# Performance work log

Measured on AMD Instinct MI355X. Metric: run time of the kernel, lower is better.

The kernel has to match this reference:

```python
import jax, jax.numpy as jnp
import numpy as np

B, D, FV, EMB, HID, E = 256, 1000, 300, 128, 128, 32000
NUM_LAYERS = 3


def _gcn_layer(h, src, tgt, W, b):
    # PyG GCNConv (add_self_loops=True, normalize=True) over N = h.shape[0] nodes.
    # NOTE: edges only reference nodes [0, D) (faithful to original forward),
    # but self-loops exist for all N nodes.
    N = h.shape[0]
    h = h @ W.T  # [N, out]
    deg = jnp.ones((N,), h.dtype).at[tgt].add(1.0)  # self-loop + in-degree
    dinv = deg ** -0.5
    coef = dinv[src] * dinv[tgt]  # [E]
    agg = jnp.zeros_like(h).at[tgt].add(h[src] * coef[:, None])
    agg = agg + h * (dinv * dinv)[:, None]  # self-loop messages
    return agg + b


def setup_inputs() -> dict:
    key = jax.random.key(0)
    ks = jax.random.split(key, 10)
    inp = {
        "X_num": jax.random.normal(ks[0], (B, 800), jnp.float32),
        "X_cat": jax.random.normal(ks[1], (B, 200), jnp.float32),
        "V": jax.random.normal(ks[2], (D, FV), jnp.float32),
        "edge_index": jax.random.randint(ks[3], (2, E), 0, D, jnp.int32),
        "W_embed": jax.random.normal(ks[4], (EMB, FV), jnp.float32) / np.sqrt(FV),
        "b_embed": jnp.zeros((EMB,), jnp.float32),
        "W0": jax.random.normal(ks[5], (HID, EMB), jnp.float32) / np.sqrt(EMB),
        "b0": jnp.zeros((HID,), jnp.float32),
        "W1": jax.random.normal(ks[6], (HID, HID), jnp.float32) / np.sqrt(HID),
        "b1": jnp.zeros((HID,), jnp.float32),
        "W2": jax.random.normal(ks[7], (HID, HID), jnp.float32) / np.sqrt(HID),
        "b2": jnp.zeros((HID,), jnp.float32),
    }
    return inp


def reference(X_num, X_cat, V, edge_index, W_embed, b_embed, W0, b0, W1, b1, W2, b2):
    x = jnp.concatenate([X_num, X_cat], axis=1)  # [B, D]
    emb = V @ W_embed.T + b_embed  # [D, EMB]
    h = x[:, :, None] * emb[None, :, :]  # [B, D, EMB]
    h = h.reshape(B * D, EMB)
    src, tgt = edge_index[0], edge_index[1]
    for W, b in ((W0, b0), (W1, b1), (W2, b2)):
        h = jax.nn.relu(_gcn_layer(h, src, tgt, W, b))
    h = h.reshape(B, D, HID)
    return h.mean(axis=1)  # conv_pool_method == 'mean'
```

## Files before the change

### kernel.cpp

```cpp
#include <hip/hip_runtime.h>

#define B_N 256
#define D_N 1000
#define H_N 128
#define E_N 32000
#define CAP 128

typedef unsigned int uint32;
typedef unsigned short u16;
typedef __attribute__((ext_vector_type(8))) short bf16x8;
typedef __attribute__((ext_vector_type(4))) float f32x4;

__device__ __forceinline__ u16 f2bf(float f) {
    union { float f; uint32 u; } v; v.f = f;
    return (u16)((v.u + 0x7fffu + ((v.u >> 16) & 1u)) >> 16);
}
__device__ __forceinline__ float bf2f(u16 h) {
    union { uint32 u; float f; } v; v.u = ((uint32)h) << 16;
    return v.f;
}

__global__ void k_setup(const float* __restrict__ V, const float* __restrict__ W_embed,
                        const float* __restrict__ b_embed, const int* __restrict__ eidx,
                        const float* __restrict__ W1, const float* __restrict__ W2,
                        int* deg, int* __restrict__ es,
                        u16* __restrict__ w1h, u16* __restrict__ w2h,
                        float* __restrict__ emb) {
    int bid = blockIdx.x, tid = threadIdx.x;
    if (bid < 500) {
        __shared__ float sV[600];
        for (int i = tid; i < 600; i += 256) sV[i] = V[bid * 600 + i];
        __syncthreads();
        int half = tid >> 7, e = tid & 127;
        int d = bid * 2 + half;
        const float4* wr = (const float4*)(W_embed + e * 300);
        const float4* vv = (const float4*)(sV + half * 300);
        float s = b_embed[e];
#pragma unroll 5
        for (int f = 0; f < 75; ++f) {
            float4 w = wr[f], x = vv[f];
            s += w.x * x.x + w.y * x.y + w.z * x.z + w.w * x.w;
        }
        emb[d * H_N + e] = s;
    } else if (bid < 625) {
        int e = (bid - 500) * 256 + tid;
        if (e < E_N) {
            int s = eidx[e], t = eidx[E_N + e];
            int pos = atomicAdd(&deg[t], 1);
            if (pos < CAP) es[t * CAP + pos] = s;
        }
    } else {
        int i = (bid - 625) * 256 + tid;
        if (i < H_N * H_N) { w1h[i] = f2bf(W1[i]); w2h[i] = f2bf(W2[i]); }
    }
}

__global__ void k_e1(const float* __restrict__ emb, const float* __restrict__ W0,
                     const float* __restrict__ Xn, const float* __restrict__ Xc,
                     const int* __restrict__ deg, u16* __restrict__ E1h,
                     float* __restrict__ t0, float* __restrict__ dinv) {
    __shared__ float se[256];
    int tid = threadIdx.x, bid = blockIdx.x;
    se[tid] = emb[bid * 256 + tid];
    if (tid < 2) {
        int dd = bid * 2 + tid;
        dinv[dd] = rsqrtf(1.0f + (float)deg[dd]);
    }
    __syncthreads();
    int half = tid >> 7, e = tid & 127;
    int d = bid * 2 + half;
    const float4* er = (const float4*)(se + half * 128);
    const float4* wr = (const float4*)(W0 + e * 128);
    float s = 0.f;
#pragma unroll 8
    for (int k = 0; k < 32; ++k) {
        float4 a = er[k], w = wr[k];
        s += a.x * w.x + a.y * w.y + a.z * w.z + a.w * w.w;
    }
    E1h[d * H_N + e] = f2bf(s);
    float x0 = (d < 800) ? Xn[d] : Xc[d - 800];
    t0[d * H_N + e] = x0 * s;
}

__global__ void k_layer(const float* __restrict__ t_in, const float* __restrict__ bias,
                        const float* __restrict__ Wn, const int* __restrict__ deg,
                        const int* __restrict__ es, const float* __restrict__ dinv,
                        float* __restrict__ t_out, float* out, int pool) {
    __shared__ float sh[128];
    int d = blockIdx.x, e = threadIdx.x;
    float di = dinv[d];
    float acc = t_in[d * H_N + e] * di * di;
    int n = deg[d]; if (n > CAP) n = CAP;
    const int* row = es + d * CAP;
    for (int i = 0; i < n; ++i) {
        int s = row[i];
        acc += di * dinv[s] * t_in[s * H_N + e];
    }
    float h = acc + bias[e];
    h = h > 0.f ? h : 0.f;
    if (pool) { atomicAdd(&out[e], h * (1.0f / 1000.0f)); return; }
    sh[e] = h;
    __syncthreads();
    const float4* hr = (const float4*)sh;
    const float4* wr = (const float4*)(Wn + e * 128);
    float s = 0.f;
#pragma unroll 8
    for (int k = 0; k < 32; ++k) {
        float4 a = hr[k], w = wr[k];
        s += a.x * w.x + a.y * w.y + a.z * w.z + a.w * w.w;
    }
    t_out[d * H_N + e] = s;
}

__device__ __forceinline__ int swzo(int row, int col) {
    return row * 128 + ((((col >> 3) ^ (row & 7))) << 3) + (col & 7);
}

__global__ __launch_bounds__(256, 1)
void k_big(const float* __restrict__ Xn, const float* __restrict__ Xc,
           const u16* __restrict__ E1h, const u16* __restrict__ w1h,
           const u16* __restrict__ w2h, const float* __restrict__ b0,
           const float* __restrict__ b1, const float* __restrict__ b2,
           float* __restrict__ out) {
    __shared__ __align__(16) u16 sH[4 * 32 * 128];
    const int tid = threadIdx.x;
    const int wave = tid >> 6, lane = tid & 63;
    const int quad = lane >> 4, l15 = lane & 15;
    const int bi = 1 + blockIdx.x;
    u16* wbase = sH + wave * (32 * 128);

    bf16x8 w1f[8][4], w2f[8][4];
#pragma unroll
    for (int n = 0; n < 8; ++n)
#pragma unroll
        for (int ks = 0; ks < 4; ++ks) {
            int off = (n * 16 + l15) * 128 + (ks * 4 + quad) * 8;
            w1f[n][ks] = *(const bf16x8*)(w1h + off);
            w2f[n][ks] = *(const bf16x8*)(w2h + off);
        }

    uint32 b0p[4][4];
#pragma unroll
    for (int ks = 0; ks < 4; ++ks) {
        const float* bp = b0 + (ks * 4 + quad) * 8;
#pragma unroll
        for (int q = 0; q < 4; ++q)
            b0p[ks][q] = (uint32)f2bf(bp[2 * q]) | ((uint32)f2bf(bp[2 * q + 1]) << 16);
    }
    float b1g[8], b2g[8];
#pragma unroll
    for (int n = 0; n < 8; ++n) { b1g[n] = b1[n * 16 + l15]; b2g[n] = b2[n * 16 + l15]; }

    float accO[8];
#pragma unroll
    for (int n = 0; n < 8; ++n) accO[n] = 0.f;

    const int odd = l15 & 1;

    for (int c = 0; c < 8; ++c) {
        int tile = wave * 8 + c;
        int mbase = tile * 32;

        float xv[2];
#pragma unroll
        for (int rt = 0; rt < 2; ++rt) {
            int m = mbase + rt * 16 + l15;
            int mc = m < D_N ? m : D_N - 1;
            xv[rt] = (mc < 800) ? Xn[bi * 800 + mc] : Xc[bi * 200 + (mc - 800)];
        }

        uint4 e1r[4][2];
#pragma unroll
        for (int ks = 0; ks < 4; ++ks)
#pragma unroll
            for (int rt = 0; rt < 2; ++rt) {
                int m = mbase + rt * 16 + l15;
                int mc = m < D_N ? m : D_N - 1;
                e1r[ks][rt] = *(const uint4*)(E1h + mc * H_N + (ks * 4 + quad) * 8);
            }

        f32x4 acc[2][8];
#pragma unroll
        for (int rt = 0; rt < 2; ++rt)
#pragma unroll
            for (int n = 0; n < 8; ++n) { acc[rt][n][0] = 0.f; acc[rt][n][1] = 0.f; acc[rt][n][2] = 0.f; acc[rt][n][3] = 0.f; }

#pragma unroll
        for (int ks = 0; ks < 4; ++ks) {
            bf16x8 a[2];
#pragma unroll
            for (int rt = 0; rt < 2; ++rt) {
                const u16* ep = (const u16*)&e1r[ks][rt];
                bf16x8 av;
#pragma unroll
                for (int j = 0; j < 8; ++j) {
                    float bb = bf2f((u16)((b0p[ks][j >> 1] >> ((j & 1) * 16)) & 0xffffu));
                    float h = xv[rt] * bf2f(ep[j]) + bb;
                    h = h > 0.f ? h : 0.f;
                    av[j] = (short)f2bf(h);
                }
                a[rt] = av;
            }
#pragma unroll
            for (int n = 0; n < 8; ++n) {
                acc[0][n] = __builtin_amdgcn_mfma_f32_16x16x32_bf16(a[0], w1f[n][ks], acc[0][n], 0, 0, 0);
                acc[1][n] = __builtin_amdgcn_mfma_f32_16x16x32_bf16(a[1], w1f[n][ks], acc[1][n], 0, 0, 0);
            }
        }

#pragma unroll
        for (int rt = 0; rt < 2; ++rt)
#pragma unroll
            for (int n = 0; n < 8; ++n) {
                float v0 = acc[rt][n][0] + b1g[n]; v0 = v0 > 0.f ? v0 : 0.f;
                float v1 = acc[rt][n][1] + b1g[n]; v1 = v1 > 0.f ? v1 : 0.f;
                float v2 = acc[rt][n][2] + b1g[n]; v2 = v2 > 0.f ? v2 : 0.f;
                float v3 = acc[rt][n][3] + b1g[n]; v3 = v3 > 0.f ? v3 : 0.f;
                float t0 = __shfl_xor(v0, 1), t1 = __shfl_xor(v1, 1);
                float t2 = __shfl_xor(v2, 1), t3 = __shfl_xor(v3, 1);
                float lo0 = odd ? t2 : v0, hi0 = odd ? v2 : t0;
                float lo1 = odd ? t3 : v1, hi1 = odd ? v3 : t1;
                int rA = rt * 16 + quad * 4 + (odd ? 2 : 0);
                int ce = n * 16 + (l15 & ~1);
                uint32 p0 = (uint32)f2bf(lo0) | ((uint32)f2bf(hi0) << 16);
                uint32 p1 = (uint32)f2bf(lo1) | ((uint32)f2bf(hi1) << 16);
                *(uint32*)&wbase[swzo(rA, ce)] = p0;
                *(uint32*)&wbase[swzo(rA + 1, ce)] = p1;
            }
        __syncthreads();

#pragma unroll
        for (int rt = 0; rt < 2; ++rt)
#pragma unroll
            for (int n = 0; n < 8; ++n) { acc[rt][n][0] = 0.f; acc[rt][n][1] = 0.f; acc[rt][n][2] = 0.f; acc[rt][n][3] = 0.f; }
#pragma unroll
        for (int ks = 0; ks < 4; ++ks) {
            bf16x8 a2[2];
#pragma unroll
            for (int rt = 0; rt < 2; ++rt) {
                int r = rt * 16 + l15;
                a2[rt] = *(const bf16x8*)&wbase[r * 128 + (((ks * 4 + quad) ^ (r & 7)) << 3)];
            }
#pragma unroll
            for (int n = 0; n < 8; ++n) {
                acc[0][n] = __builtin_amdgcn_mfma_f32_16x16x32_bf16(a2[0], w2f[n][ks], acc[0][n], 0, 0, 0);
                acc[1][n] = __builtin_amdgcn_mfma_f32_16x16x32_bf16(a2[1], w2f[n][ks], acc[1][n], 0, 0, 0);
            }
        }

        int rem = D_N - mbase;
#pragma unroll
        for (int rt = 0; rt < 2; ++rt)
#pragma unroll
            for (int n = 0; n < 8; ++n)
#pragma unroll
                for (int i = 0; i < 4; ++i) {
                    int row32 = rt * 16 + quad * 4 + i;
                    float v = acc[rt][n][i] + b2g[n];
                    v = v > 0.f ? v : 0.f;
                    if (row32 < rem) accO[n] += v;
                }
        __syncthreads();
    }

#pragma unroll
    for (int n = 0; n < 8; ++n) {
        float cs = accO[n];
        cs += __shfl_xor(cs, 16);
        cs += __shfl_xor(cs, 32);
        if (lane < 16) atomicAdd(&out[bi * H_N + n * 16 + l15], cs * (1.0f / 1000.0f));
    }
}

extern "C" void kernel_launch(void* const* d_in, const int* in_sizes, int n_in,
                              void* d_out, int out_size, void* d_ws, size_t ws_size,
                              hipStream_t stream) {
    const float* Xn = (const float*)d_in[0];
    const float* Xc = (const float*)d_in[1];
    const float* V = (const float*)d_in[2];
    const int* eidx = (const int*)d_in[3];
    const float* W_embed = (const float*)d_in[4];
    const float* b_embed = (const float*)d_in[5];
    const float* W0 = (const float*)d_in[6];
    const float* b0 = (const float*)d_in[7];
    const float* W1 = (const float*)d_in[8];
    const float* b1 = (const float*)d_in[9];
    const float* W2 = (const float*)d_in[10];
    const float* b2 = (const float*)d_in[11];
    float* out = (float*)d_out;

    char* p = (char*)d_ws;
    auto alloc = [&](size_t bytes) -> char* {
        char* r = p;
        p += (bytes + 255) & ~(size_t)255;
        return r;
    };
    float* emb  = (float*)alloc(D_N * H_N * 4);
    u16*   E1h  = (u16*)  alloc(D_N * H_N * 2);
    float* t0   = (float*)alloc(D_N * H_N * 4);
    float* t1   = (float*)alloc(D_N * H_N * 4);
    float* t2   = (float*)alloc(D_N * H_N * 4);
    u16*   w1h  = (u16*)  alloc(H_N * H_N * 2);
    u16*   w2h  = (u16*)  alloc(H_N * H_N * 2);
    float* dinv = (float*)alloc(D_N * 4);
    int*   deg  = (int*)  alloc(D_N * 4);
    int*   es   = (int*)  alloc(D_N * CAP * 4);

    hipMemsetAsync(deg, 0, D_N * 4, stream);
    hipMemsetAsync(out, 0, B_N * H_N * 4, stream);

    k_setup<<<dim3(689), dim3(256), 0, stream>>>(V, W_embed, b_embed, eidx, W1, W2,
                                                 deg, es, w1h, w2h, emb);
    k_e1<<<dim3(500), dim3(256), 0, stream>>>(emb, W0, Xn, Xc, deg, E1h, t0, dinv);
    k_big<<<dim3(255), dim3(256), 0, stream>>>(Xn, Xc, E1h, w1h, w2h, b0, b1, b2, out);
    k_layer<<<dim3(1000), dim3(128), 0, stream>>>(t0, b0, W1, deg, es, dinv, t1, out, 0);
    k_layer<<<dim3(1000), dim3(128), 0, stream>>>(t1, b1, W2, deg, es, dinv, t2, out, 0);
    k_layer<<<dim3(1000), dim3(128), 0, stream>>>(t2, b2, (const float*)nullptr, deg, es, dinv,
                                                  (float*)nullptr, out, 1);
}
```

Measured before the change: 222.2 us.

## Fuse setup and E1 kernels, split big kernel across two blocks per batch

Merges the embedding, W0 projection, edge bucketing, weight conversion and output zeroing into one prep kernel, which removes a launch and the memset of out. The layer kernel computes the inverse-sqrt degree inline and unrolls the neighbor gather by four. k_big now runs two blocks per batch row with a 2-blocks-per-CU launch bound. It keeps W1 in swizzled LDS and reads W2 fragments from global memory instead of holding both weight matrices in registers, and it drops the per-chunk barrier. This trades register pressure for more occupancy and parallelism, at the cost of repeated global or LDS reads of the weights.

```diff
diff --git a/kernel.cpp b/kernel.cpp
--- a/kernel.cpp
+++ b/kernel.cpp
@@ -1,4 +1,5 @@
 #include <hip/hip_runtime.h>
+#include <hip/hip_bf16.h>
 
 #define B_N 256
 #define D_N 1000
@@ -15,86 +16,98 @@
     union { float f; uint32 u; } v; v.f = f;
     return (u16)((v.u + 0x7fffu + ((v.u >> 16) & 1u)) >> 16);
 }
-__device__ __forceinline__ float bf2f(u16 h) {
-    union { uint32 u; float f; } v; v.u = ((uint32)h) << 16;
-    return v.f;
-}
-
-__global__ void k_setup(const float* __restrict__ V, const float* __restrict__ W_embed,
-                        const float* __restrict__ b_embed, const int* __restrict__ eidx,
-                        const float* __restrict__ W1, const float* __restrict__ W2,
-                        int* deg, int* __restrict__ es,
-                        u16* __restrict__ w1h, u16* __restrict__ w2h,
-                        float* __restrict__ emb) {
+__device__ __forceinline__ float asf(uint32 u) {
+    union { uint32 u; float f; } v; v.u = u; return v.f;
+}
+
+__global__ void k_prep(const float* __restrict__ V, const float* __restrict__ W_embed,
+                       const float* __restrict__ b_embed, const int* __restrict__ eidx,
+                       const float* __restrict__ W0,
+                       const float* __restrict__ Xn, const float* __restrict__ Xc,
+                       const float* __restrict__ W1, const float* __restrict__ W2,
+                       int* deg, int* __restrict__ es,
+                       u16* __restrict__ w1h, u16* __restrict__ w2h,
+                       u16* __restrict__ E1h, float* __restrict__ t0,
+                       float* __restrict__ out) {
     int bid = blockIdx.x, tid = threadIdx.x;
-    if (bid < 500) {
-        __shared__ float sV[600];
-        for (int i = tid; i < 600; i += 256) sV[i] = V[bid * 600 + i];
-        __syncthreads();
-        int half = tid >> 7, e = tid & 127;
-        int d = bid * 2 + half;
+    if (bid < 125) {
+        __shared__ float sEmb[8 * 128];
+        int e = tid & 127, h = tid >> 7;
+        int d0 = bid * 8 + h * 4;
         const float4* wr = (const float4*)(W_embed + e * 300);
-        const float4* vv = (const float4*)(sV + half * 300);
-        float s = b_embed[e];
+        float s0 = b_embed[e], s1 = s0, s2 = s0, s3 = s0;
 #pragma unroll 5
         for (int f = 0; f < 75; ++f) {
-            float4 w = wr[f], x = vv[f];
-            s += w.x * x.x + w.y * x.y + w.z * x.z + w.w * x.w;
-        }
-        emb[d * H_N + e] = s;
-    } else if (bid < 625) {
-        int e = (bid - 500) * 256 + tid;
-        if (e < E_N) {
-            int s = eidx[e], t = eidx[E_N + e];
-            int pos = atomicAdd(&deg[t], 1);
-            if (pos < CAP) es[t * CAP + pos] = s;
-        }
+            float4 w = wr[f];
+            float4 v0 = *(const float4*)(V + (d0 + 0) * 300 + f * 4);
+            float4 v1 = *(const float4*)(V + (d0 + 1) * 300 + f * 4);
+            float4 v2 = *(const float4*)(V + (d0 + 2) * 300 + f * 4);
+            float4 v3 = *(const float4*)(V + (d0 + 3) * 300 + f * 4);
+            s0 += w.x * v0.x + w.y * v0.y + w.z * v0.z + w.w * v0.w;
+            s1 += w.x * v1.x + w.y * v1.y + w.z * v1.z + w.w * v1.w;
+            s2 += w.x * v2.x + w.y * v2.y + w.z * v2.z + w.w * v2.w;
+            s3 += w.x * v3.x + w.y * v3.y + w.z * v3.z + w.w * v3.w;
+        }
+        sEmb[(h * 4 + 0) * 128 + e] = s0;
+        sEmb[(h * 4 + 1) * 128 + e] = s1;
+        sEmb[(h * 4 + 2) * 128 + e] = s2;
+        sEmb[(h * 4 + 3) * 128 + e] = s3;
+        __syncthreads();
+        const float4* w0r = (const float4*)(W0 + e * 128);
+        float t[4] = {0.f, 0.f, 0.f, 0.f};
+#pragma unroll 8
+        for (int k = 0; k < 32; ++k) {
+            float4 w = w0r[k];
+#pragma unroll
+            for (int p = 0; p < 4; ++p) {
+                float4 em = *(const float4*)&sEmb[(h * 4 + p) * 128 + k * 4];
+                t[p] += w.x * em.x + w.y * em.y + w.z * em.z + w.w * em.w;
+            }
+        }
+#pragma unroll
+        for (int p = 0; p < 4; ++p) {
+            int d = d0 + p;
+            float x0 = (d < 800) ? Xn[d] : Xc[d - 800];
+            E1h[d * H_N + e] = f2bf(t[p]);
+            t0[d * H_N + e] = x0 * t[p];
+        }
+    } else if (bid < 250) {
+        int i = (bid - 125) * 256 + tid;
+        int s = eidx[i], t = eidx[E_N + i];
+        int pos = atomicAdd(&deg[t], 1);
+        if (pos < CAP) es[t * CAP + pos] = s;
+    } else if (bid < 314) {
+        int i = (bid - 250) * 256 + tid;
+        w1h[i] = f2bf(W1[i]); w2h[i] = f2bf(W2[i]);
     } else {
-        int i = (bid - 625) * 256 + tid;
-        if (i < H_N * H_N) { w1h[i] = f2bf(W1[i]); w2h[i] = f2bf(W2[i]); }
-    }
-}
-
-__global__ void k_e1(const float* __restrict__ emb, const float* __restrict__ W0,
-                     const float* __restrict__ Xn, const float* __restrict__ Xc,
-                     const int* __restrict__ deg, u16* __restrict__ E1h,
-                     float* __restrict__ t0, float* __restrict__ dinv) {
-    __shared__ float se[256];
-    int tid = threadIdx.x, bid = blockIdx.x;
-    se[tid] = emb[bid * 256 + tid];
-    if (tid < 2) {
-        int dd = bid * 2 + tid;
-        dinv[dd] = rsqrtf(1.0f + (float)deg[dd]);
-    }
-    __syncthreads();
-    int half = tid >> 7, e = tid & 127;
-    int d = bid * 2 + half;
-    const float4* er = (const float4*)(se + half * 128);
-    const float4* wr = (const float4*)(W0 + e * 128);
-    float s = 0.f;
-#pragma unroll 8
-    for (int k = 0; k < 32; ++k) {
-        float4 a = er[k], w = wr[k];
-        s += a.x * w.x + a.y * w.y + a.z * w.z + a.w * w.w;
-    }
-    E1h[d * H_N + e] = f2bf(s);
-    float x0 = (d < 800) ? Xn[d] : Xc[d - 800];
-    t0[d * H_N + e] = x0 * s;
+        int i = (bid - 314) * 256 + tid;
+        out[i] = 0.f;
+    }
 }
 
 __global__ void k_layer(const float* __restrict__ t_in, const float* __restrict__ bias,
                         const float* __restrict__ Wn, const int* __restrict__ deg,
-                        const int* __restrict__ es, const float* __restrict__ dinv,
+                        const int* __restrict__ es,
                         float* __restrict__ t_out, float* out, int pool) {
     __shared__ float sh[128];
     int d = blockIdx.x, e = threadIdx.x;
-    float di = dinv[d];
+    float di = rsqrtf(1.f + (float)deg[d]);
     float acc = t_in[d * H_N + e] * di * di;
     int n = deg[d]; if (n > CAP) n = CAP;
     const int* row = es + d * CAP;
-    for (int i = 0; i < n; ++i) {
+    int i = 0;
+    for (; i + 4 <= n; i += 4) {
+        int a0 = row[i], a1 = row[i + 1], a2 = row[i + 2], a3 = row[i + 3];
+        float c0 = rsqrtf(1.f + (float)deg[a0]);
+        float c1 = rsqrtf(1.f + (float)deg[a1]);
+        float c2 = rsqrtf(1.f + (float)deg[a2]);
+        float c3 = rsqrtf(1.f + (float)deg[a3]);
+        acc += di * (c0 * t_in[a0 * H_N + e] + c1 * t_in[a1 * H_N + e] +
+                     c2 * t_in[a2 * H_N + e] + c3 * t_in[a3 * H_N + e]);
+    }
+    for (; i < n; ++i) {
         int s = row[i];
-        acc += di * dinv[s] * t_in[s * H_N + e];
+        acc += di * rsqrtf(1.f + (float)deg[s]) * t_in[s * H_N + e];
     }
     float h = acc + bias[e];
     h = h > 0.f ? h : 0.f;
@@ -112,155 +125,158 @@
     t_out[d * H_N + e] = s;
 }
 
-__device__ __forceinline__ int swzo(int row, int col) {
-    return row * 128 + ((((col >> 3) ^ (row & 7))) << 3) + (col & 7);
-}
-
-__global__ __launch_bounds__(256, 1)
+__device__ __forceinline__ int swz(int row, int col8) {
+    return row * 128 + ((col8 ^ (row & 7)) << 3);
+}
+
+__global__ __launch_bounds__(256, 2)
 void k_big(const float* __restrict__ Xn, const float* __restrict__ Xc,
            const u16* __restrict__ E1h, const u16* __restrict__ w1h,
            const u16* __restrict__ w2h, const float* __restrict__ b0,
            const float* __restrict__ b1, const float* __restrict__ b2,
            float* __restrict__ out) {
-    __shared__ __align__(16) u16 sH[4 * 32 * 128];
+    __shared__ __align__(16) u16 sW1[128 * 128];
+    __shared__ __align__(16) u16 sT[4 * 32 * 128];
+
     const int tid = threadIdx.x;
     const int wave = tid >> 6, lane = tid & 63;
     const int quad = lane >> 4, l15 = lane & 15;
-    const int bi = 1 + blockIdx.x;
-    u16* wbase = sH + wave * (32 * 128);
-
-    bf16x8 w1f[8][4], w2f[8][4];
-#pragma unroll
-    for (int n = 0; n < 8; ++n)
+    const int bi = 1 + (blockIdx.x >> 1);
+    const int half = blockIdx.x & 1;
+    u16* tw = sT + wave * (32 * 128);
+    const int odd = l15 & 1;
+
+    {
+        const uint4* src = (const uint4*)w1h;
+        for (int i = tid; i < 2048; i += 256) {
+            int row = i >> 4, g = i & 15;
+            *(uint4*)&sW1[swz(row, g)] = src[i];
+        }
+    }
+
+    float b0v[4][8];
+#pragma unroll
+    for (int ks = 0; ks < 4; ++ks) {
+        float4 lo = *(const float4*)(b0 + (ks * 4 + quad) * 8);
+        float4 hi = *(const float4*)(b0 + (ks * 4 + quad) * 8 + 4);
+        b0v[ks][0] = lo.x; b0v[ks][1] = lo.y; b0v[ks][2] = lo.z; b0v[ks][3] = lo.w;
+        b0v[ks][4] = hi.x; b0v[ks][5] = hi.y; b0v[ks][6] = hi.z; b0v[ks][7] = hi.w;
+    }
+    float b1g[8], b2g[8];
+#pragma unroll
+    for (int n = 0; n < 8; ++n) { b1g[n] = b1[n * 16 + l15]; b2g[n] = b2[n * 16 + l15]; }
+
+    __syncthreads();
+
+    float accO[8];
+#pragma unroll
+    for (int n = 0; n < 8; ++n) accO[n] = 0.f;
+
+    for (int c = 0; c < 4; ++c) {
+        int mbase = half * 512 + wave * 128 + c * 32;
+        int rA = mbase + l15;      int rAc = rA < D_N ? rA : D_N - 1;
+        int rB = rA + 16;          int rBc = rB < D_N ? rB : D_N - 1;
+        float xvA = (rAc < 800) ? Xn[bi * 800 + rAc] : Xc[bi * 200 + rAc - 800];
+        float xvB = (rBc < 800) ? Xn[bi * 800 + rBc] : Xc[bi * 200 + rBc - 800];
+
+        uint4 eA[4], eB[4];
 #pragma unroll
         for (int ks = 0; ks < 4; ++ks) {
-            int off = (n * 16 + l15) * 128 + (ks * 4 + quad) * 8;
-            w1f[n][ks] = *(const bf16x8*)(w1h + off);
-            w2f[n][ks] = *(const bf16x8*)(w2h + off);
-        }
-
-    uint32 b0p[4][4];
-#pragma unroll
-    for (int ks = 0; ks < 4; ++ks) {
-        const float* bp = b0 + (ks * 4 + quad) * 8;
-#pragma unroll
-        for (int q = 0; q < 4; ++q)
-            b0p[ks][q] = (uint32)f2bf(bp[2 * q]) | ((uint32)f2bf(bp[2 * q + 1]) << 16);
-    }
-    float b1g[8], b2g[8];
-#pragma unroll
-    for (int n = 0; n < 8; ++n) { b1g[n] = b1[n * 16 + l15]; b2g[n] = b2[n * 16 + l15]; }
-
-    float accO[8];
-#pragma unroll
-    for (int n = 0; n < 8; ++n) accO[n] = 0.f;
-
-    const int odd = l15 & 1;
-
-    for (int c = 0; c < 8; ++c) {
-        int tile = wave * 8 + c;
-        int mbase = tile * 32;
-
-        float xv[2];
+            eA[ks] = *(const uint4*)(E1h + rAc * H_N + (ks * 4 + quad) * 8);
+            eB[ks] = *(const uint4*)(E1h + rBc * H_N + (ks * 4 + quad) * 8);
+        }
+
+        f32x4 acc0[8], acc1[8];
+#pragma unroll
+        for (int n = 0; n < 8; ++n) {
+            acc0[n][0] = 0.f; acc0[n][1] = 0.f; acc0[n][2] = 0.f; acc0[n][3] = 0.f;
+            acc1[n][0] = 0.f; acc1[n][1] = 0.f; acc1[n][2] = 0.f; acc1[n][3] = 0.f;
+        }
+
+#pragma unroll
+        for (int ks = 0; ks < 4; ++ks) {
+            const uint32* pA = (const uint32*)&eA[ks];
+            const uint32* pB = (const uint32*)&eB[ks];
+            bf16x8 aA, aB;
+#pragma unroll
+            for (int p = 0; p < 4; ++p) {
+                uint32 uA = pA[p], uB = pB[p];
+                float hA0 = fmaf(xvA, asf(uA << 16), b0v[ks][2 * p]);
+                float hA1 = fmaf(xvA, asf(uA & 0xffff0000u), b0v[ks][2 * p + 1]);
+                float hB0 = fmaf(xvB, asf(uB << 16), b0v[ks][2 * p]);
+                float hB1 = fmaf(xvB, asf(uB & 0xffff0000u), b0v[ks][2 * p + 1]);
+                hA0 = hA0 > 0.f ? hA0 : 0.f;  hA1 = hA1 > 0.f ? hA1 : 0.f;
+                hB0 = hB0 > 0.f ? hB0 : 0.f;  hB1 = hB1 > 0.f ? hB1 : 0.f;
+                aA[2 * p] = (short)f2bf(hA0); aA[2 * p + 1] = (short)f2bf(hA1);
+                aB[2 * p] = (short)f2bf(hB0); aB[2 * p + 1] = (short)f2bf(hB1);
+            }
+#pragma unroll
+            for (int n = 0; n < 8; ++n) {
+                bf16x8 bw = *(const bf16x8*)&sW1[swz(n * 16 + l15, ks * 4 + quad)];
+                acc0[n] = __builtin_amdgcn_mfma_f32_16x16x32_bf16(aA, bw, acc0[n], 0, 0, 0);
+                acc1[n] = __builtin_amdgcn_mfma_f32_16x16x32_bf16(aB, bw, acc1[n], 0, 0, 0);
+            }
+        }
+
 #pragma unroll
         for (int rt = 0; rt < 2; ++rt) {
-            int m = mbase + rt * 16 + l15;
-            int mc = m < D_N ? m : D_N - 1;
-            xv[rt] = (mc < 800) ? Xn[bi * 800 + mc] : Xc[bi * 200 + (mc - 800)];
-        }
-
-        uint4 e1r[4][2];
-#pragma unroll
-        for (int ks = 0; ks < 4; ++ks)
-#pragma unroll
-            for (int rt = 0; rt < 2; ++rt) {
-                int m = mbase + rt * 16 + l15;
-                int mc = m < D_N ? m : D_N - 1;
-                e1r[ks][rt] = *(const uint4*)(E1h + mc * H_N + (ks * 4 + quad) * 8);
-            }
-
-        f32x4 acc[2][8];
-#pragma unroll
-        for (int rt = 0; rt < 2; ++rt)
-#pragma unroll
-            for (int n = 0; n < 8; ++n) { acc[rt][n][0] = 0.f; acc[rt][n][1] = 0.f; acc[rt][n][2] = 0.f; acc[rt][n][3] = 0.f; }
-
-#pragma unroll
-        for (int ks = 0; ks < 4; ++ks) {
-            bf16x8 a[2];
-#pragma unroll
-            for (int rt = 0; rt < 2; ++rt) {
-                const u16* ep = (const u16*)&e1r[ks][rt];
-                bf16x8 av;
-#pragma unroll
-                for (int j = 0; j < 8; ++j) {
-                    float bb = bf2f((u16)((b0p[ks][j >> 1] >> ((j & 1) * 16)) & 0xffffu));
-                    float h = xv[rt] * bf2f(ep[j]) + bb;
-                    h = h > 0.f ? h : 0.f;
-                    av[j] = (short)f2bf(h);
-                }
-                a[rt] = av;
-            }
 #pragma unroll
             for (int n = 0; n < 8; ++n) {
-                acc[0][n] = __builtin_amdgcn_mfma_f32_16x16x32_bf16(a[0], w1f[n][ks], acc[0][n], 0, 0, 0);
-                acc[1][n] = __builtin_amdgcn_mfma_f32_16x16x32_bf16(a[1], w1f[n][ks], acc[1][n], 0, 0, 0);
-            }
-        }
-
-#pragma unroll
-        for (int rt = 0; rt < 2; ++rt)
-#pragma unroll
-            for (int n = 0; n < 8; ++n) {
-                float v0 = acc[rt][n][0] + b1g[n]; v0 = v0 > 0.f ? v0 : 0.f;
-                float v1 = acc[rt][n][1] + b1g[n]; v1 = v1 > 0.f ? v1 : 0.f;
-                float v2 = acc[rt][n][2] + b1g[n]; v2 = v2 > 0.f ? v2 : 0.f;
-                float v3 = acc[rt][n][3] + b1g[n]; v3 = v3 > 0.f ? v3 : 0.f;
-                float t0 = __shfl_xor(v0, 1), t1 = __shfl_xor(v1, 1);
-                float t2 = __shfl_xor(v2, 1), t3 = __shfl_xor(v3, 1);
-                float lo0 = odd ? t2 : v0, hi0 = odd ? v2 : t0;
-                float lo1 = odd ? t3 : v1, hi1 = odd ? v3 : t1;
-                int rA = rt * 16 + quad * 4 + (odd ? 2 : 0);
+                f32x4 a = rt ? acc1[n] : acc0[n];
+                float v0 = a[0] + b1g[n]; v0 = v0 > 0.f ? v0 : 0.f;
+                float v1 = a[1] + b1g[n]; v1 = v1 > 0.f ? v1 : 0.f;
+                float v2 = a[2] + b1g[n]; v2 = v2 > 0.f ? v2 : 0.f;
+                float v3 = a[3] + b1g[n]; v3 = v3 > 0.f ? v3 : 0.f;
+                float t0_ = __shfl_xor(v0, 1), t1_ = __shfl_xor(v1, 1);
+                float t2_ = __shfl_xor(v2, 1), t3_ = __shfl_xor(v3, 1);
+                float lo0 = odd ? t2_ : v0, hi0 = odd ? v2 : t0_;
+                float lo1 = odd ? t3_ : v1, hi1 = odd ? v3 : t1_;
+                int r0 = rt * 16 + quad * 4 + (odd ? 2 : 0);
                 int ce = n * 16 + (l15 & ~1);
                 uint32 p0 = (uint32)f2bf(lo0) | ((uint32)f2bf(hi0) << 16);
                 uint32 p1 = (uint32)f2bf(lo1) | ((uint32)f2bf(hi1) << 16);
-                *(uint32*)&wbase[swzo(rA, ce)] = p0;
-                *(uint32*)&wbase[swzo(rA + 1, ce)] = p1;
-            }
-        __syncthreads();
-
-#pragma unroll
-        for (int rt = 0; rt < 2; ++rt)
-#pragma unroll
-            for (int n = 0; n < 8; ++n) { acc[rt][n][0] = 0.f; acc[rt][n][1] = 0.f; acc[rt][n][2] = 0.f; acc[rt][n][3] = 0.f; }
+                int base0 = r0 * 128 + (((ce >> 3) ^ (r0 & 7)) << 3) + (ce & 7);
+                int r1 = r0 + 1;
+                int base1 = r1 * 128 + (((ce >> 3) ^ (r1 & 7)) << 3) + (ce & 7);
+                *(uint32*)&tw[base0] = p0;
+                *(uint32*)&tw[base1] = p1;
+            }
+        }
+
+#pragma unroll
+        for (int n = 0; n < 8; ++n) {
+            acc0[n][0] = 0.f; acc0[n][1] = 0.f; acc0[n][2] = 0.f; acc0[n][3] = 0.f;
+            acc1[n][0] = 0.f; acc1[n][1] = 0.f; acc1[n][2] = 0.f; acc1[n][3] = 0.f;
+        }
 #pragma unroll
         for (int ks = 0; ks < 4; ++ks) {
-            bf16x8 a2[2];
-#pragma unroll
-            for (int rt = 0; rt < 2; ++rt) {
-                int r = rt * 16 + l15;
-                a2[rt] = *(const bf16x8*)&wbase[r * 128 + (((ks * 4 + quad) ^ (r & 7)) << 3)];
-            }
+            int k8 = ks * 4 + quad;
+            int ra = l15, rb = 16 + l15;
+            bf16x8 a2A = *(const bf16x8*)&tw[ra * 128 + ((k8 ^ (ra & 7)) << 3)];
+            bf16x8 a2B = *(const bf16x8*)&tw[rb * 128 + ((k8 ^ (rb & 7)) << 3)];
 #pragma unroll
             for (int n = 0; n < 8; ++n) {
-                acc[0][n] = __builtin_amdgcn_mfma_f32_16x16x32_bf16(a2[0], w2f[n][ks], acc[0][n], 0, 0, 0);
-                acc[1][n] = __builtin_amdgcn_mfma_f32_16x16x32_bf16(a2[1], w2f[n][ks], acc[1][n], 0, 0, 0);
+                bf16x8 bw = *(const bf16x8*)(w2h + (n * 16 + l15) * H_N + k8 * 8);
+                acc0[n] = __builtin_amdgcn_mfma_f32_16x16x32_bf16(a2A, bw, acc0[n], 0, 0, 0);
+                acc1[n] = __builtin_amdgcn_mfma_f32_16x16x32_bf16(a2B, bw, acc1[n], 0, 0, 0);
             }
         }
 
         int rem = D_N - mbase;
 #pragma unroll
-        for (int rt = 0; rt < 2; ++rt)
-#pragma unroll
-            for (int n = 0; n < 8; ++n)
+        for (int rt = 0; rt < 2; ++rt) {
+#pragma unroll
+            for (int n = 0; n < 8; ++n) {
+                f32x4 a = rt ? acc1[n] : acc0[n];
 #pragma unroll
                 for (int i = 0; i < 4; ++i) {
                     int row32 = rt * 16 + quad * 4 + i;
-                    float v = acc[rt][n][i] + b2g[n];
+                    float v = a[i] + b2g[n];
                     v = v > 0.f ? v : 0.f;
                     if (row32 < rem) accO[n] += v;
                 }
-        __syncthreads();
+            }
+        }
     }
 
 #pragma unroll
@@ -295,26 +311,23 @@
         p += (bytes + 255) & ~(size_t)255;
         return r;
     };
-    float* emb  = (float*)alloc(D_N * H_N * 4);
-    u16*   E1h  = (u16*)  alloc(D_N * H_N * 2);
-    float* t0   = (float*)alloc(D_N * H_N * 4);
-    float* t1   = (float*)alloc(D_N * H_N * 4);
-    float* t2   = (float*)alloc(D_N * H_N * 4);
-    u16*   w1h  = (u16*)  alloc(H_N * H_N * 2);
-    u16*   w2h  = (u16*)  alloc(H_N * H_N * 2);
-    float* dinv = (float*)alloc(D_N * 4);
-    int*   deg  = (int*)  alloc(D_N * 4);
-    int*   es   = (int*)  alloc(D_N * CAP * 4);
+    u16*   E1h = (u16*)  alloc(D_N * H_N * 2);
+    float* t0  = (float*)alloc(D_N * H_N * 4);
+    float* t1  = (float*)alloc(D_N * H_N * 4);
+    float* t2  = (float*)alloc(D_N * H_N * 4);
+    u16*   w1h = (u16*)  alloc(H_N * H_N * 2);
+    u16*   w2h = (u16*)  alloc(H_N * H_N * 2);
+    int*   deg = (int*)  alloc(D_N * 4);
+    int*   es  = (int*)  alloc(D_N * CAP * 4);
 
     hipMemsetAsync(deg, 0, D_N * 4, stream);
-    hipMemsetAsync(out, 0, B_N * H_N * 4, stream);
-
-    k_setup<<<dim3(689), dim3(256), 0, stream>>>(V, W_embed, b_embed, eidx, W1, W2,
-                                                 deg, es, w1h, w2h, emb);
-    k_e1<<<dim3(500), dim3(256), 0, stream>>>(emb, W0, Xn, Xc, deg, E1h, t0, dinv);
-    k_big<<<dim3(255), dim3(256), 0, stream>>>(Xn, Xc, E1h, w1h, w2h, b0, b1, b2, out);
-    k_layer<<<dim3(1000), dim3(128), 0, stream>>>(t0, b0, W1, deg, es, dinv, t1, out, 0);
-    k_layer<<<dim3(1000), dim3(128), 0, stream>>>(t1, b1, W2, deg, es, dinv, t2, out, 0);
-    k_layer<<<dim3(1000), dim3(128), 0, stream>>>(t2, b2, (const float*)nullptr, deg, es, dinv,
+
+    k_prep<<<dim3(442), dim3(256), 0, stream>>>(V, W_embed, b_embed, eidx, W0,
+                                                Xn, Xc, W1, W2, deg, es,
+                                                w1h, w2h, E1h, t0, out);
+    k_big<<<dim3(510), dim3(256), 0, stream>>>(Xn, Xc, E1h, w1h, w2h, b0, b1, b2, out);
+    k_layer<<<dim3(1000), dim3(128), 0, stream>>>(t0, b0, W1, deg, es, t1, out, 0);
+    k_layer<<<dim3(1000), dim3(128), 0, stream>>>(t1, b1, W2, deg, es, t2, out, 0);
+    k_layer<<<dim3(1000), dim3(128), 0, stream>>>(t2, b2, (const float*)nullptr, deg, es,
                                                   (float*)nullptr, out, 1);
 }
```

Result: slower. 275.0 us (+23.8%).
